# Optimization experiments

Measured on AMD Instinct MI355X. Metric: run time of the kernel, lower is better.

Reference implementation:

```python
import jax, jax.numpy as jnp
import numpy as np

B, N, G = 16, 6000, 256
T = 200                     # TRAIN_ROIS_PER_IMAGE
RATIO = 0.33                # POSITIVE_ROI_RATIO
POS_NUM = int(T * RATIO)    # 66 positive slots
NEG_SLOTS = T - POS_NUM     # 134 negative slots
BBOX_STD = jnp.asarray([0.1, 0.1, 0.2, 0.2], jnp.float32)
EPS = 1e-8


def _rand_boxes(key, b, n):
    # valid [y1,x1,y2,x2] boxes in [0,1]
    k1, k2 = jax.random.split(key)
    tl = jax.random.uniform(k1, (b, n, 2)) * 0.7
    wh = jax.random.uniform(k2, (b, n, 2)) * 0.25 + 0.02
    return jnp.concatenate([tl, tl + wh], axis=-1).astype(jnp.float32)


def setup_inputs() -> dict:
    key = jax.random.key(0)
    k1, k2, k3, k4, k5 = jax.random.split(key, 5)
    rois = _rand_boxes(k1, B, N)
    rois = rois.at[:, N - 1000:].set(0.0)          # zero padding tail (remove_zero_padding)
    gt_boxes = _rand_boxes(k2, B, G)
    gt_ids = jax.random.randint(k3, (B, G), 1, 81, dtype=jnp.int32)
    gt_ids = gt_ids.at[:, G - 32:G - 16].set(-1)   # crowd boxes (ids < 0)
    gt_ids = gt_ids.at[:, G - 16:].set(0)          # padded gt
    gt_boxes = gt_boxes.at[:, G - 16:].set(0.0)
    pos_score = jax.random.uniform(k4, (B, N), dtype=jnp.float32)
    neg_score = jax.random.uniform(k5, (B, N), dtype=jnp.float32)
    return {"rois": rois, "gt_ids": gt_ids, "gt_boxes": gt_boxes,
            "pos_score": pos_score, "neg_score": neg_score}


def _pairwise_iou(a, b):
    # a:[N,4], b:[G,4] -> [N,G]
    y1 = jnp.maximum(a[:, None, 0], b[None, :, 0])
    x1 = jnp.maximum(a[:, None, 1], b[None, :, 1])
    y2 = jnp.minimum(a[:, None, 2], b[None, :, 2])
    x2 = jnp.minimum(a[:, None, 3], b[None, :, 3])
    inter = jnp.clip(y2 - y1, 0.0) * jnp.clip(x2 - x1, 0.0)
    area_a = (a[:, 2] - a[:, 0]) * (a[:, 3] - a[:, 1])
    area_b = (b[:, 2] - b[:, 0]) * (b[:, 3] - b[:, 1])
    union = area_a[:, None] + area_b[None, :] - inter
    return inter / jnp.maximum(union, EPS)


def _bbox_offset(boxes, gt):
    h = jnp.maximum(boxes[:, 2] - boxes[:, 0], EPS)
    w = jnp.maximum(boxes[:, 3] - boxes[:, 1], EPS)
    cy = boxes[:, 0] + 0.5 * h
    cx = boxes[:, 1] + 0.5 * w
    gh = jnp.maximum(gt[:, 2] - gt[:, 0], EPS)
    gw = jnp.maximum(gt[:, 3] - gt[:, 1], EPS)
    gcy = gt[:, 0] + 0.5 * gh
    gcx = gt[:, 1] + 0.5 * gw
    off = jnp.stack([(gcy - cy) / h, (gcx - cx) / w,
                     jnp.log(gh / h), jnp.log(gw / w)], axis=1)
    return off / BBOX_STD


def _per_image(rois, gt_ids, gt_boxes, pos_score, neg_score):
    roi_valid = jnp.any(rois != 0.0, axis=1)        # [N]
    gt_valid = jnp.any(gt_boxes != 0.0, axis=1)     # [G]
    crowd = gt_valid & (gt_ids < 0)
    non_crowd = gt_valid & (gt_ids > 0)

    iou = _pairwise_iou(rois, gt_boxes)             # [N,G]
    iou_nc = jnp.where(non_crowd[None, :], iou, -1.0)
    iou_nc_max = jnp.max(iou_nc, axis=1)
    iou_cr_max = jnp.max(jnp.where(crowd[None, :], iou, 0.0), axis=1)

    pos_mask = roi_valid & (iou_nc_max >= 0.5)
    neg_mask = roi_valid & (iou_nc_max < 0.5) & (iou_cr_max < 0.001)

    # random sampling == sort by iid uniform scores (masked out -> -inf)
    pos_idx = jnp.argsort(-jnp.where(pos_mask, pos_score, -jnp.inf))[:POS_NUM]
    pos_count = jnp.minimum(jnp.sum(pos_mask), POS_NUM).astype(jnp.int32)
    pos_slot_valid = jnp.arange(POS_NUM) < pos_count

    neg_target = (jnp.float32(1.0 / RATIO) * pos_count.astype(jnp.float32)).astype(jnp.int32) - pos_count
    neg_idx = jnp.argsort(-jnp.where(neg_mask, neg_score, -jnp.inf))[:NEG_SLOTS]
    neg_count = jnp.minimum(jnp.sum(neg_mask).astype(jnp.int32),
                            jnp.minimum(neg_target, NEG_SLOTS))
    neg_slot_valid = jnp.arange(NEG_SLOTS) < neg_count

    pos_rois_raw = rois[pos_idx]                                   # [P,4]
    pos_rois = jnp.where(pos_slot_valid[:, None], pos_rois_raw, 0.0)
    neg_rois = jnp.where(neg_slot_valid[:, None], rois[neg_idx], 0.0)

    assign = jnp.argmax(iou_nc[pos_idx], axis=1)                   # gt assignment
    roi_gt_boxes = gt_boxes[assign]
    roi_gt_ids = jnp.where(pos_slot_valid, gt_ids[assign], 0)

    off = _bbox_offset(pos_rois_raw, roi_gt_boxes)
    off = jnp.where(pos_slot_valid[:, None], off, 0.0)

    out_rois = jnp.concatenate([pos_rois, neg_rois], axis=0)       # [T,4]
    out_ids = jnp.pad(roi_gt_ids, (0, NEG_SLOTS))                  # [T]
    out_off = jnp.pad(off, ((0, NEG_SLOTS), (0, 0)))               # [T,4]
    return out_rois, out_ids, out_off


def reference(rois, gt_ids, gt_boxes, pos_score, neg_score):
    return jax.vmap(_per_image)(rois, gt_ids, gt_boxes, pos_score, neg_score)
```

## Files before the change

kernel.cpp:

```cpp
#include <hip/hip_runtime.h>

#define BIMG 16
#define NROI 6000
#define NGT  256
#define TPOS 66
#define TNEG 134
#define TTOT 200
#define EPSF 1e-8f
#define INVALID_SCORE 0xFFFFFFFFu

#define RPB 128
#define UNITSB 47
#define P1_BLOCKS (UNITSB * BIMG)
#define NWAIT (2 * BIMG)
#define NT 256
#define VSLOTS 6
#define CAND_CAP 384

#define MAGIC1 0x9E3779B9u
#define MAGIC2 0x85EBCA77u

typedef unsigned long long u64;
typedef unsigned int u32;
typedef unsigned short u16;

struct P1Shared {
    float4 ncbox[NGT];
    float  ncarea[NGT];
    float4 crbox[NGT];
    float  crarea[NGT];
    u16    gmap[NGT];
    int    wnc[4], wcr[4];
    int    poscnt;
};

struct SelShared {
    u32 hist[2048];
    u32 wtot[4];
    u32 wsuf[4];
    int pick;
    u32 higher;
    u32 pickpop;
    u32 count;
    u64 comp[CAND_CAP];
    int cnt;
    int sel[TNEG];
};

__device__ __forceinline__ void phase1_block(
    int unit,
    const float* __restrict__ rois, const int* __restrict__ gt_ids,
    const float* __restrict__ gt_boxes, const float* __restrict__ pos_score,
    const float* __restrict__ neg_score, u32* __restrict__ pos_s,
    u32* __restrict__ neg_s, u32* __restrict__ assign, u32* __restrict__ flags,
    P1Shared& S)
{
#pragma clang fp contract(off)
    const int b = unit / UNITSB;
    const int u = unit - b * UNITSB;
    const int tid = threadIdx.x;
    const int sub = tid & 1;
    const int r   = tid >> 1;

    if (tid == 0) S.poscnt = 0;

    const int n = u * RPB + r;
    const int ne = min(n, NROI - 1);
    const float4 rb = ((const float4*)rois)[b * NROI + ne];
    float ps_in = 0.f, ns_in = 0.f;
    if (sub == 0) {
        ps_in = pos_score[b * NROI + ne];
        ns_in = neg_score[b * NROI + ne];
    }

    {
        const int g = tid;
        const int lane = g & 63, w = g >> 6;
        float4 gb = ((const float4*)gt_boxes)[b * NGT + g];
        bool valid = (gb.x != 0.f) || (gb.y != 0.f) || (gb.z != 0.f) || (gb.w != 0.f);
        int id = gt_ids[b * NGT + g];
        float area = (gb.z - gb.x) * (gb.w - gb.y);
        bool isnc = valid && (id > 0);
        bool iscr = valid && (id < 0);
        u64 mnc = __ballot(isnc);
        u64 mcr = __ballot(iscr);
        if (lane == 0) { S.wnc[w] = (int)__popcll(mnc); S.wcr[w] = (int)__popcll(mcr); }
        __syncthreads();
        int offnc = 0, offcr = 0;
        for (int j = 0; j < w; ++j) { offnc += S.wnc[j]; offcr += S.wcr[j]; }
        u64 below = (lane == 0) ? 0ull : (~0ull >> (64 - lane));
        if (isnc) {
            int slot = offnc + (int)__popcll(mnc & below);
            S.ncbox[slot] = gb;
            S.ncarea[slot] = area;
            S.gmap[slot] = (u16)g;
        }
        if (iscr) {
            int slot = offcr + (int)__popcll(mcr & below);
            S.crbox[slot] = gb;
            S.crarea[slot] = area;
        }
    }
    __syncthreads();
    const int nccnt = S.wnc[0] + S.wnc[1] + S.wnc[2] + S.wnc[3];
    const int crcnt = S.wcr[0] + S.wcr[1] + S.wcr[2] + S.wcr[3];

    const bool rvalid = (rb.x != 0.f) || (rb.y != 0.f) || (rb.z != 0.f) || (rb.w != 0.f);
    float best = -1.0f;
    int   bsl  = 0;
    float crmax = 0.0f;

    if (rvalid) {
        const float area_a = (rb.z - rb.x) * (rb.w - rb.y);
        const int h  = nccnt >> 1;
        const int i0 = sub ? h : 0;
        const int i1 = sub ? nccnt : h;
#pragma unroll 4
        for (int i = i0; i < i1; ++i) {
            float4 p0 = S.ncbox[i];
            float  ab = S.ncarea[i];
            float y1 = fmaxf(rb.x, p0.x);
            float x1 = fmaxf(rb.y, p0.y);
            float y2 = fminf(rb.z, p0.z);
            float x2 = fminf(rb.w, p0.w);
            float ih = fmaxf(y2 - y1, 0.0f);
            float iw = fmaxf(x2 - x1, 0.0f);
            float inter = ih * iw;
            float uni = fmaxf(area_a + ab - inter, EPSF);
            float iou = inter / uni;
            if (iou > best) { best = iou; bsl = i; }
        }
        const int hc  = crcnt >> 1;
        const int c0i = sub ? hc : 0;
        const int c1i = sub ? crcnt : hc;
#pragma unroll 4
        for (int i = c0i; i < c1i; ++i) {
            float4 p0 = S.crbox[i];
            float  ab = S.crarea[i];
            float y1 = fmaxf(rb.x, p0.x);
            float x1 = fmaxf(rb.y, p0.y);
            float y2 = fminf(rb.z, p0.z);
            float x2 = fminf(rb.w, p0.w);
            float ih = fmaxf(y2 - y1, 0.0f);
            float iw = fmaxf(x2 - x1, 0.0f);
            float inter = ih * iw;
            float uni = fmaxf(area_a + ab - inter, EPSF);
            crmax = fmaxf(crmax, inter / uni);
        }
        float ov = __shfl_xor(best, 1);
        int   os = __shfl_xor(bsl, 1);
        float oc = __shfl_xor(crmax, 1);
        if ((ov > best) || ((ov == best) && (os < bsl))) { best = ov; bsl = os; }
        crmax = fmaxf(crmax, oc);
    }

    u32 ps = INVALID_SCORE, ns = INVALID_SCORE;
    if (rvalid && n < NROI) {
        if (best >= 0.5f)
            ps = __float_as_uint(ps_in);
        if ((best < 0.5f) && (crmax < 0.001f))
            ns = __float_as_uint(ns_in);
    }
    {
        u64 pb = __ballot((sub == 0) && (ps != INVALID_SCORE));
        if ((tid & 63) == 0) atomicAdd(&S.poscnt, (int)__popcll(pb));
    }
    if (sub == 0 && n < NROI) {
        int gsel = (nccnt > 0) ? (int)S.gmap[bsl] : 0;
        __hip_atomic_store(&pos_s[b * NROI + n], ps,
                           __ATOMIC_RELAXED, __HIP_MEMORY_SCOPE_AGENT);
        __hip_atomic_store(&neg_s[b * NROI + n], ns,
                           __ATOMIC_RELAXED, __HIP_MEMORY_SCOPE_AGENT);
        __hip_atomic_store(&assign[b * NROI + n], (u32)gsel,
                           __ATOMIC_RELAXED, __HIP_MEMORY_SCOPE_AGENT);
    }

    __syncthreads();
    if (tid == 0) {
        u32 cnt = (u32)S.poscnt;
        __hip_atomic_store(&flags[2 * unit],     MAGIC1 ^ cnt,
                           __ATOMIC_RELAXED, __HIP_MEMORY_SCOPE_AGENT);
        __hip_atomic_store(&flags[2 * unit + 1], MAGIC2 ^ cnt,
                           __ATOMIC_RELAXED, __HIP_MEMORY_SCOPE_AGENT);
    }
}

__device__ __forceinline__ int radix_select(const u32* __restrict__ src, int K,
                                            int tid, int lane, int w, SelShared* S)
{
    const uint4* src4 = (const uint4*)src;
    int myvalid = 0;
#pragma unroll
    for (int s = 0; s < VSLOTS; ++s) {
        int vi = s * NT + tid;
        uint4 v = src4[vi];
        int base = vi * 4;
        myvalid += (base + 0 < NROI && v.x != INVALID_SCORE);
        myvalid += (base + 1 < NROI && v.y != INVALID_SCORE);
        myvalid += (base + 2 < NROI && v.z != INVALID_SCORE);
        myvalid += (base + 3 < NROI && v.w != INVALID_SCORE);
    }
    for (int off = 1; off < 64; off <<= 1) myvalid += __shfl_xor(myvalid, off);
    if (tid == 0) S->count = 0;
    __syncthreads();
    if (lane == 0) atomicAdd(&S->count, (u32)myvalid);
    __syncthreads();
    const int total = (int)S->count;
    const int K0 = min(K, total);
    if (K0 <= 0) return total;

    int Krem = K0;
    u64 prefix = 0ull, mask = 0ull;
    int cand = total;

    for (int p = 3; p >= 0; --p) {
        if (cand <= CAND_CAP) break;
        const int shift = p * 11;
        for (int i = tid; i < 2048; i += NT) S->hist[i] = 0;
        __syncthreads();
#pragma unroll
        for (int s = 0; s < VSLOTS; ++s) {
            int vi = s * NT + tid;
            uint4 v = src4[vi];
            int base = vi * 4;
            u32 vv[4] = {v.x, v.y, v.z, v.w};
#pragma unroll
            for (int j = 0; j < 4; ++j) {
                int idx = base + j;
                if (idx < NROI && vv[j] != INVALID_SCORE) {
                    u64 kk = ((u64)vv[j] << 13) | (u64)(8191 - idx);
                    if ((kk & mask) == prefix)
                        atomicAdd(&S->hist[(u32)(kk >> shift) & 2047u], 1u);
                }
            }
        }
        __syncthreads();
        u32 local = 0;
#pragma unroll
        for (int j = 0; j < 8; ++j) local += S->hist[8 * tid + j];
        u32 suf = local;
        for (int off = 1; off < 64; off <<= 1) {
            u32 v = __shfl_down(suf, off);
            if (lane + off < 64) suf += v;
        }
        if (lane == 0) S->wtot[w] = suf;
        __syncthreads();
        if (tid < 4) {
            u32 t = 0;
            for (int j = tid + 1; j < 4; ++j) t += S->wtot[j];
            S->wsuf[tid] = t;
        }
        __syncthreads();
        u32 Sincl = suf + S->wsuf[w];
        for (int k2 = 0; k2 < 8; ++k2) {
            u32 h = S->hist[8 * tid + k2];
            u32 Snext = Sincl - h;
            if (Sincl >= (u32)Krem && Snext < (u32)Krem) {
                S->pick = 8 * tid + k2;
                S->higher = Snext;
                S->pickpop = h;
            }
            Sincl = Snext;
        }
        __syncthreads();
        prefix |= ((u64)(u32)S->pick) << shift;
        mask   |= (2047ull << shift);
        Krem   -= (int)S->higher;
        cand    = (K0 - Krem) + (int)S->pickpop;
        __syncthreads();
    }

    if (tid == 0) S->cnt = 0;
    __syncthreads();
#pragma unroll
    for (int s = 0; s < VSLOTS; ++s) {
        int vi = s * NT + tid;
        uint4 v = src4[vi];
        int base = vi * 4;
        u32 vv[4] = {v.x, v.y, v.z, v.w};
#pragma unroll
        for (int j = 0; j < 4; ++j) {
            int idx = base + j;
            if (idx < NROI && vv[j] != INVALID_SCORE) {
                u64 kk = ((u64)vv[j] << 13) | (u64)(8191 - idx);
                if ((kk & mask) >= prefix) {
                    int pos = atomicAdd(&S->cnt, 1);
                    S->comp[pos] = kk;
                }
            }
        }
    }
    __syncthreads();
    const int Cnt = S->cnt;
    const int CntP = (Cnt + 15) & ~15;
    for (int i = Cnt + tid; i < CntP; i += NT) S->comp[i] = 0ull;
    __syncthreads();
    for (int c0 = tid; c0 < Cnt; c0 += NT) {
        u64 kk = S->comp[c0];
        int rank = 0;
        for (int j = 0; j < CntP; j += 16) {
            int r16 = 0;
#pragma unroll
            for (int q = 0; q < 16; ++q) r16 += (S->comp[j + q] > kk);
            rank += r16;
        }
        if (rank < K0) S->sel[rank] = 8191 - (int)(kk & 8191ull);
    }
    __syncthreads();
    return total;
}

__device__ __forceinline__ void phase2_block(
    int wbid,
    const float* __restrict__ rois, const int* __restrict__ gt_ids,
    const float* __restrict__ gt_boxes, const u32* __restrict__ pos_s,
    const u32* __restrict__ neg_s, const u32* __restrict__ assign,
    const u32* __restrict__ flags, float* __restrict__ out, SelShared& S)
{
#pragma clang fp contract(off)
    __shared__ int s_ndone;
    __shared__ int s_psum;
    const int b = wbid >> 1;
    const int side = wbid & 1;
    const int tid = threadIdx.x;
    const int lane = tid & 63;
    const int w = tid >> 6;

    const u32* fb = flags + 2 * (b * UNITSB);
    int mydone = (tid < UNITSB) ? 0 : 1;
    int mycnt = 0;
    for (;;) {
        if (tid == 0) s_ndone = 0;
        __syncthreads();
        if (!mydone) {
            u32 a = __hip_atomic_load(&fb[2 * tid],
                                      __ATOMIC_RELAXED, __HIP_MEMORY_SCOPE_AGENT);
            u32 c = __hip_atomic_load(&fb[2 * tid + 1],
                                      __ATOMIC_RELAXED, __HIP_MEMORY_SCOPE_AGENT);
            u32 ca = a ^ MAGIC1, cb = c ^ MAGIC2;
            if (ca == cb && ca <= (u32)RPB) { mydone = 1; mycnt = (int)ca; }
        }
        int d = mydone;
        for (int off = 1; off < 64; off <<= 1) d += __shfl_xor(d, off);
        if (lane == 0) atomicAdd(&s_ndone, d);
        __syncthreads();
        if (s_ndone == NT) break;
        __builtin_amdgcn_s_sleep(8);
    }
    if (tid == 0) {
        (void)__hip_atomic_load(&fb[0], __ATOMIC_ACQUIRE, __HIP_MEMORY_SCOPE_AGENT);
        s_psum = 0;
    }
    __syncthreads();
    if (tid < UNITSB && mycnt) atomicAdd(&s_psum, mycnt);
    __syncthreads();
    const int pos_total = s_psum;

    float* out_rois = out;
    float* out_ids  = out + BIMG * TTOT * 4;
    float* out_off  = out + BIMG * TTOT * 4 + BIMG * TTOT;

    if (side == 0) {
        radix_select(pos_s + (size_t)b * NROI, TPOS, tid, lane, w, &S);
        const int pos_count = min(pos_total, TPOS);

        if (tid < TPOS) {
            const int base = b * TTOT + tid;
            float4 ro  = make_float4(0.f, 0.f, 0.f, 0.f);
            float  idv = 0.f;
            float4 off = make_float4(0.f, 0.f, 0.f, 0.f);
            if (tid < pos_count) {
                int nn = S.sel[tid];
                float4 rb = ((const float4*)rois)[b * NROI + nn];
                ro = rb;
                int g = (int)assign[b * NROI + nn];
                float4 gb = ((const float4*)gt_boxes)[b * NGT + g];
                idv = (float)gt_ids[b * NGT + g];

                float h  = fmaxf(rb.z - rb.x, EPSF);
                float wd = fmaxf(rb.w - rb.y, EPSF);
                float cy = rb.x + 0.5f * h;
                float cx = rb.y + 0.5f * wd;
                float gh = fmaxf(gb.z - gb.x, EPSF);
                float gw = fmaxf(gb.w - gb.y, EPSF);
                float gcy = gb.x + 0.5f * gh;
                float gcx = gb.y + 0.5f * gw;
                off.x = ((gcy - cy) / h)  / 0.1f;
                off.y = ((gcx - cx) / wd) / 0.1f;
                off.z = logf(gh / h)  / 0.2f;
                off.w = logf(gw / wd) / 0.2f;
            }
            ((float4*)out_rois)[base] = ro;
            out_ids[base] = idv;
            ((float4*)out_off)[base] = off;
        }
    } else {
        const int pos_count = min(pos_total, TPOS);
        const float ratio_inv = (float)(1.0 / 0.33);
        const int neg_target = (int)(ratio_inv * (float)pos_count) - pos_count;

        const int neg_total = radix_select(neg_s + (size_t)b * NROI, TNEG,
                                           tid, lane, w, &S);
        const int neg_count = max(0, min(neg_total, min(neg_target, TNEG)));

        if (tid < TNEG) {
            const int base = b * TTOT + TPOS + tid;
            float4 ro = make_float4(0.f, 0.f, 0.f, 0.f);
            if (tid < neg_count) {
                int nn = S.sel[tid];
                ro = ((const float4*)rois)[b * NROI + nn];
            }
            ((float4*)out_rois)[base] = ro;
            out_ids[base] = 0.f;
            ((float4*)out_off)[base] = make_float4(0.f, 0.f, 0.f, 0.f);
        }
    }
}

__global__ __launch_bounds__(NT, 4)
void fused_kernel(const float* __restrict__ rois,
                  const int* __restrict__ gt_ids,
                  const float* __restrict__ gt_boxes,
                  const float* __restrict__ pos_score,
                  const float* __restrict__ neg_score,
                  u32* __restrict__ pos_s,
                  u32* __restrict__ neg_s,
                  u32* __restrict__ assign,
                  u32* __restrict__ flags,
                  float* __restrict__ out)
{
    constexpr size_t SB = sizeof(P1Shared) > sizeof(SelShared)
                        ? sizeof(P1Shared) : sizeof(SelShared);
    __shared__ __align__(16) char smem[SB];

    if (blockIdx.x >= NWAIT) {
        phase1_block((int)blockIdx.x - NWAIT, rois, gt_ids, gt_boxes, pos_score,
                     neg_score, pos_s, neg_s, assign, flags,
                     *reinterpret_cast<P1Shared*>(smem));
    } else {
        phase2_block((int)blockIdx.x, rois, gt_ids, gt_boxes,
                     pos_s, neg_s, assign, flags, out,
                     *reinterpret_cast<SelShared*>(smem));
    }
}

extern "C" void kernel_launch(void* const* d_in, const int* in_sizes, int n_in,
                              void* d_out, int out_size, void* d_ws, size_t ws_size,
                              hipStream_t stream) {
    const float* rois      = (const float*)d_in[0];
    const int*   gt_ids    = (const int*)d_in[1];
    const float* gt_boxes  = (const float*)d_in[2];
    const float* pos_score = (const float*)d_in[3];
    const float* neg_score = (const float*)d_in[4];
    float* out = (float*)d_out;

    char* ws = (char*)d_ws;
    u32* pos_s  = (u32*)(ws + 0);
    u32* neg_s  = (u32*)(ws + 384000);
    u32* assign = (u32*)(ws + 768000);
    u32* flags  = (u32*)(ws + 1152000);

    fused_kernel<<<NWAIT + P1_BLOCKS, NT, 0, stream>>>(
        rois, gt_ids, gt_boxes, pos_score, neg_score,
        pos_s, neg_s, assign, flags, out);
}
```

Before: 94.33 us.

## Fold selection phase into last two phase-1 blocks per image, drop dedicated waiters

Removes the 32 separate waiter blocks. The last two phase-1 blocks of each image now run their own IoU work first, then spin on the flags and perform the positive/negative radix selection. This frees the slots that waiter blocks held while spinning, and cuts shared memory by recomputing gt areas inline. In exchange the selection starts only after those final blocks finish their phase-1 work, and it relies on all blocks of an image being co-resident to avoid deadlock.

```diff
diff --git a/kernel.cpp b/kernel.cpp
--- a/kernel.cpp
+++ b/kernel.cpp
@@ -12,7 +12,6 @@
 #define RPB 128
 #define UNITSB 47
 #define P1_BLOCKS (UNITSB * BIMG)
-#define NWAIT (2 * BIMG)
 #define NT 256
 #define VSLOTS 6
 #define CAND_CAP 384
@@ -26,9 +25,7 @@
 
 struct P1Shared {
     float4 ncbox[NGT];
-    float  ncarea[NGT];
     float4 crbox[NGT];
-    float  crarea[NGT];
     u16    gmap[NGT];
     int    wnc[4], wcr[4];
     int    poscnt;
@@ -47,18 +44,157 @@
     int sel[TNEG];
 };
 
-__device__ __forceinline__ void phase1_block(
-    int unit,
-    const float* __restrict__ rois, const int* __restrict__ gt_ids,
-    const float* __restrict__ gt_boxes, const float* __restrict__ pos_score,
-    const float* __restrict__ neg_score, u32* __restrict__ pos_s,
-    u32* __restrict__ neg_s, u32* __restrict__ assign, u32* __restrict__ flags,
-    P1Shared& S)
+__device__ __forceinline__ int radix_select(const u32* __restrict__ src, int K,
+                                            int tid, int lane, int w, SelShared* S)
+{
+    const uint4* src4 = (const uint4*)src;
+    int myvalid = 0;
+#pragma unroll
+    for (int s = 0; s < VSLOTS; ++s) {
+        int vi = s * NT + tid;
+        uint4 v = src4[vi];
+        int base = vi * 4;
+        myvalid += (base + 0 < NROI && v.x != INVALID_SCORE);
+        myvalid += (base + 1 < NROI && v.y != INVALID_SCORE);
+        myvalid += (base + 2 < NROI && v.z != INVALID_SCORE);
+        myvalid += (base + 3 < NROI && v.w != INVALID_SCORE);
+    }
+    for (int off = 1; off < 64; off <<= 1) myvalid += __shfl_xor(myvalid, off);
+    if (tid == 0) S->count = 0;
+    __syncthreads();
+    if (lane == 0) atomicAdd(&S->count, (u32)myvalid);
+    __syncthreads();
+    const int total = (int)S->count;
+    const int K0 = min(K, total);
+    if (K0 <= 0) return total;
+
+    int Krem = K0;
+    u64 prefix = 0ull, mask = 0ull;
+    int cand = total;
+
+    for (int p = 3; p >= 0; --p) {
+        if (cand <= CAND_CAP) break;
+        const int shift = p * 11;
+        for (int i = tid; i < 2048; i += NT) S->hist[i] = 0;
+        __syncthreads();
+#pragma unroll
+        for (int s = 0; s < VSLOTS; ++s) {
+            int vi = s * NT + tid;
+            uint4 v = src4[vi];
+            int base = vi * 4;
+            u32 vv[4] = {v.x, v.y, v.z, v.w};
+#pragma unroll
+            for (int j = 0; j < 4; ++j) {
+                int idx = base + j;
+                if (idx < NROI && vv[j] != INVALID_SCORE) {
+                    u64 kk = ((u64)vv[j] << 13) | (u64)(8191 - idx);
+                    if ((kk & mask) == prefix)
+                        atomicAdd(&S->hist[(u32)(kk >> shift) & 2047u], 1u);
+                }
+            }
+        }
+        __syncthreads();
+        u32 local = 0;
+#pragma unroll
+        for (int j = 0; j < 8; ++j) local += S->hist[8 * tid + j];
+        u32 suf = local;
+        for (int off = 1; off < 64; off <<= 1) {
+            u32 v = __shfl_down(suf, off);
+            if (lane + off < 64) suf += v;
+        }
+        if (lane == 0) S->wtot[w] = suf;
+        __syncthreads();
+        if (tid < 4) {
+            u32 t = 0;
+            for (int j = tid + 1; j < 4; ++j) t += S->wtot[j];
+            S->wsuf[tid] = t;
+        }
+        __syncthreads();
+        u32 Sincl = suf + S->wsuf[w];
+        for (int k2 = 0; k2 < 8; ++k2) {
+            u32 h = S->hist[8 * tid + k2];
+            u32 Snext = Sincl - h;
+            if (Sincl >= (u32)Krem && Snext < (u32)Krem) {
+                S->pick = 8 * tid + k2;
+                S->higher = Snext;
+                S->pickpop = h;
+            }
+            Sincl = Snext;
+        }
+        __syncthreads();
+        prefix |= ((u64)(u32)S->pick) << shift;
+        mask   |= (2047ull << shift);
+        Krem   -= (int)S->higher;
+        cand    = (K0 - Krem) + (int)S->pickpop;
+        __syncthreads();
+    }
+
+    if (tid == 0) S->cnt = 0;
+    __syncthreads();
+#pragma unroll
+    for (int s = 0; s < VSLOTS; ++s) {
+        int vi = s * NT + tid;
+        uint4 v = src4[vi];
+        int base = vi * 4;
+        u32 vv[4] = {v.x, v.y, v.z, v.w};
+#pragma unroll
+        for (int j = 0; j < 4; ++j) {
+            int idx = base + j;
+            if (idx < NROI && vv[j] != INVALID_SCORE) {
+                u64 kk = ((u64)vv[j] << 13) | (u64)(8191 - idx);
+                if ((kk & mask) >= prefix) {
+                    int pos = atomicAdd(&S->cnt, 1);
+                    S->comp[pos] = kk;
+                }
+            }
+        }
+    }
+    __syncthreads();
+    const int Cnt = S->cnt;
+    const int CntP = (Cnt + 15) & ~15;
+    for (int i = Cnt + tid; i < CntP; i += NT) S->comp[i] = 0ull;
+    __syncthreads();
+    for (int c0 = tid; c0 < Cnt; c0 += NT) {
+        u64 kk = S->comp[c0];
+        int rank = 0;
+        for (int j = 0; j < CntP; j += 16) {
+            int r16 = 0;
+#pragma unroll
+            for (int q = 0; q < 16; ++q) r16 += (S->comp[j + q] > kk);
+            rank += r16;
+        }
+        if (rank < K0) S->sel[rank] = 8191 - (int)(kk & 8191ull);
+    }
+    __syncthreads();
+    return total;
+}
+
+__global__ __launch_bounds__(NT, 4)
+void fused_kernel(const float* __restrict__ rois,
+                  const int* __restrict__ gt_ids,
+                  const float* __restrict__ gt_boxes,
+                  const float* __restrict__ pos_score,
+                  const float* __restrict__ neg_score,
+                  u32* __restrict__ pos_s,
+                  u32* __restrict__ neg_s,
+                  u32* __restrict__ assign,
+                  u32* __restrict__ flags,
+                  float* __restrict__ out)
 {
 #pragma clang fp contract(off)
+    constexpr size_t SB = sizeof(P1Shared) > sizeof(SelShared)
+                        ? sizeof(P1Shared) : sizeof(SelShared);
+    __shared__ __align__(16) char smem[SB];
+    __shared__ int s_ndone;
+    __shared__ int s_psum;
+    P1Shared& S = *reinterpret_cast<P1Shared*>(smem);
+
+    const int unit = (int)blockIdx.x;
     const int b = unit / UNITSB;
     const int u = unit - b * UNITSB;
     const int tid = threadIdx.x;
+    const int lane = tid & 63;
+    const int w = tid >> 6;
     const int sub = tid & 1;
     const int r   = tid >> 1;
 
@@ -75,11 +211,9 @@
 
     {
         const int g = tid;
-        const int lane = g & 63, w = g >> 6;
         float4 gb = ((const float4*)gt_boxes)[b * NGT + g];
         bool valid = (gb.x != 0.f) || (gb.y != 0.f) || (gb.z != 0.f) || (gb.w != 0.f);
         int id = gt_ids[b * NGT + g];
-        float area = (gb.z - gb.x) * (gb.w - gb.y);
         bool isnc = valid && (id > 0);
         bool iscr = valid && (id < 0);
         u64 mnc = __ballot(isnc);
@@ -92,13 +226,11 @@
         if (isnc) {
             int slot = offnc + (int)__popcll(mnc & below);
             S.ncbox[slot] = gb;
-            S.ncarea[slot] = area;
             S.gmap[slot] = (u16)g;
         }
         if (iscr) {
             int slot = offcr + (int)__popcll(mcr & below);
             S.crbox[slot] = gb;
-            S.crarea[slot] = area;
         }
     }
     __syncthreads();
@@ -118,7 +250,7 @@
 #pragma unroll 4
         for (int i = i0; i < i1; ++i) {
             float4 p0 = S.ncbox[i];
-            float  ab = S.ncarea[i];
+            float ab = (p0.z - p0.x) * (p0.w - p0.y);
             float y1 = fmaxf(rb.x, p0.x);
             float x1 = fmaxf(rb.y, p0.y);
             float y2 = fminf(rb.z, p0.z);
@@ -136,7 +268,7 @@
 #pragma unroll 4
         for (int i = c0i; i < c1i; ++i) {
             float4 p0 = S.crbox[i];
-            float  ab = S.crarea[i];
+            float ab = (p0.z - p0.x) * (p0.w - p0.y);
             float y1 = fmaxf(rb.x, p0.x);
             float x1 = fmaxf(rb.y, p0.y);
             float y2 = fminf(rb.z, p0.z);
@@ -163,7 +295,7 @@
     }
     {
         u64 pb = __ballot((sub == 0) && (ps != INVALID_SCORE));
-        if ((tid & 63) == 0) atomicAdd(&S.poscnt, (int)__popcll(pb));
+        if (lane == 0) atomicAdd(&S.poscnt, (int)__popcll(pb));
     }
     if (sub == 0 && n < NROI) {
         int gsel = (nccnt > 0) ? (int)S.gmap[bsl] : 0;
@@ -183,148 +315,9 @@
         __hip_atomic_store(&flags[2 * unit + 1], MAGIC2 ^ cnt,
                            __ATOMIC_RELAXED, __HIP_MEMORY_SCOPE_AGENT);
     }
-}
-
-__device__ __forceinline__ int radix_select(const u32* __restrict__ src, int K,
-                                            int tid, int lane, int w, SelShared* S)
-{
-    const uint4* src4 = (const uint4*)src;
-    int myvalid = 0;
-#pragma unroll
-    for (int s = 0; s < VSLOTS; ++s) {
-        int vi = s * NT + tid;
-        uint4 v = src4[vi];
-        int base = vi * 4;
-        myvalid += (base + 0 < NROI && v.x != INVALID_SCORE);
-        myvalid += (base + 1 < NROI && v.y != INVALID_SCORE);
-        myvalid += (base + 2 < NROI && v.z != INVALID_SCORE);
-        myvalid += (base + 3 < NROI && v.w != INVALID_SCORE);
-    }
-    for (int off = 1; off < 64; off <<= 1) myvalid += __shfl_xor(myvalid, off);
-    if (tid == 0) S->count = 0;
-    __syncthreads();
-    if (lane == 0) atomicAdd(&S->count, (u32)myvalid);
-    __syncthreads();
-    const int total = (int)S->count;
-    const int K0 = min(K, total);
-    if (K0 <= 0) return total;
-
-    int Krem = K0;
-    u64 prefix = 0ull, mask = 0ull;
-    int cand = total;
-
-    for (int p = 3; p >= 0; --p) {
-        if (cand <= CAND_CAP) break;
-        const int shift = p * 11;
-        for (int i = tid; i < 2048; i += NT) S->hist[i] = 0;
-        __syncthreads();
-#pragma unroll
-        for (int s = 0; s < VSLOTS; ++s) {
-            int vi = s * NT + tid;
-            uint4 v = src4[vi];
-            int base = vi * 4;
-            u32 vv[4] = {v.x, v.y, v.z, v.w};
-#pragma unroll
-            for (int j = 0; j < 4; ++j) {
-                int idx = base + j;
-                if (idx < NROI && vv[j] != INVALID_SCORE) {
-                    u64 kk = ((u64)vv[j] << 13) | (u64)(8191 - idx);
-                    if ((kk & mask) == prefix)
-                        atomicAdd(&S->hist[(u32)(kk >> shift) & 2047u], 1u);
-                }
-            }
-        }
-        __syncthreads();
-        u32 local = 0;
-#pragma unroll
-        for (int j = 0; j < 8; ++j) local += S->hist[8 * tid + j];
-        u32 suf = local;
-        for (int off = 1; off < 64; off <<= 1) {
-            u32 v = __shfl_down(suf, off);
-            if (lane + off < 64) suf += v;
-        }
-        if (lane == 0) S->wtot[w] = suf;
-        __syncthreads();
-        if (tid < 4) {
-            u32 t = 0;
-            for (int j = tid + 1; j < 4; ++j) t += S->wtot[j];
-            S->wsuf[tid] = t;
-        }
-        __syncthreads();
-        u32 Sincl = suf + S->wsuf[w];
-        for (int k2 = 0; k2 < 8; ++k2) {
-            u32 h = S->hist[8 * tid + k2];
-            u32 Snext = Sincl - h;
-            if (Sincl >= (u32)Krem && Snext < (u32)Krem) {
-                S->pick = 8 * tid + k2;
-                S->higher = Snext;
-                S->pickpop = h;
-            }
-            Sincl = Snext;
-        }
-        __syncthreads();
-        prefix |= ((u64)(u32)S->pick) << shift;
-        mask   |= (2047ull << shift);
-        Krem   -= (int)S->higher;
-        cand    = (K0 - Krem) + (int)S->pickpop;
-        __syncthreads();
-    }
-
-    if (tid == 0) S->cnt = 0;
-    __syncthreads();
-#pragma unroll
-    for (int s = 0; s < VSLOTS; ++s) {
-        int vi = s * NT + tid;
-        uint4 v = src4[vi];
-        int base = vi * 4;
-        u32 vv[4] = {v.x, v.y, v.z, v.w};
-#pragma unroll
-        for (int j = 0; j < 4; ++j) {
-            int idx = base + j;
-            if (idx < NROI && vv[j] != INVALID_SCORE) {
-                u64 kk = ((u64)vv[j] << 13) | (u64)(8191 - idx);
-                if ((kk & mask) >= prefix) {
-                    int pos = atomicAdd(&S->cnt, 1);
-                    S->comp[pos] = kk;
-                }
-            }
-        }
-    }
-    __syncthreads();
-    const int Cnt = S->cnt;
-    const int CntP = (Cnt + 15) & ~15;
-    for (int i = Cnt + tid; i < CntP; i += NT) S->comp[i] = 0ull;
-    __syncthreads();
-    for (int c0 = tid; c0 < Cnt; c0 += NT) {
-        u64 kk = S->comp[c0];
-        int rank = 0;
-        for (int j = 0; j < CntP; j += 16) {
-            int r16 = 0;
-#pragma unroll
-            for (int q = 0; q < 16; ++q) r16 += (S->comp[j + q] > kk);
-            rank += r16;
-        }
-        if (rank < K0) S->sel[rank] = 8191 - (int)(kk & 8191ull);
-    }
-    __syncthreads();
-    return total;
-}
-
-__device__ __forceinline__ void phase2_block(
-    int wbid,
-    const float* __restrict__ rois, const int* __restrict__ gt_ids,
-    const float* __restrict__ gt_boxes, const u32* __restrict__ pos_s,
-    const u32* __restrict__ neg_s, const u32* __restrict__ assign,
-    const u32* __restrict__ flags, float* __restrict__ out, SelShared& S)
-{
-#pragma clang fp contract(off)
-    __shared__ int s_ndone;
-    __shared__ int s_psum;
-    const int b = wbid >> 1;
-    const int side = wbid & 1;
-    const int tid = threadIdx.x;
-    const int lane = tid & 63;
-    const int w = tid >> 6;
+
+    if (u < UNITSB - 2) return;
+    const int side = (u == UNITSB - 1) ? 1 : 0;
 
     const u32* fb = flags + 2 * (b * UNITSB);
     int mydone = (tid < UNITSB) ? 0 : 1;
@@ -356,12 +349,14 @@
     __syncthreads();
     const int pos_total = s_psum;
 
+    SelShared& Q = *reinterpret_cast<SelShared*>(smem);
+
     float* out_rois = out;
     float* out_ids  = out + BIMG * TTOT * 4;
     float* out_off  = out + BIMG * TTOT * 4 + BIMG * TTOT;
 
     if (side == 0) {
-        radix_select(pos_s + (size_t)b * NROI, TPOS, tid, lane, w, &S);
+        radix_select(pos_s + (size_t)b * NROI, TPOS, tid, lane, w, &Q);
         const int pos_count = min(pos_total, TPOS);
 
         if (tid < TPOS) {
@@ -370,17 +365,17 @@
             float  idv = 0.f;
             float4 off = make_float4(0.f, 0.f, 0.f, 0.f);
             if (tid < pos_count) {
-                int nn = S.sel[tid];
-                float4 rb = ((const float4*)rois)[b * NROI + nn];
-                ro = rb;
+                int nn = Q.sel[tid];
+                float4 rb2 = ((const float4*)rois)[b * NROI + nn];
+                ro = rb2;
                 int g = (int)assign[b * NROI + nn];
                 float4 gb = ((const float4*)gt_boxes)[b * NGT + g];
                 idv = (float)gt_ids[b * NGT + g];
 
-                float h  = fmaxf(rb.z - rb.x, EPSF);
-                float wd = fmaxf(rb.w - rb.y, EPSF);
-                float cy = rb.x + 0.5f * h;
-                float cx = rb.y + 0.5f * wd;
+                float h  = fmaxf(rb2.z - rb2.x, EPSF);
+                float wd = fmaxf(rb2.w - rb2.y, EPSF);
+                float cy = rb2.x + 0.5f * h;
+                float cx = rb2.y + 0.5f * wd;
                 float gh = fmaxf(gb.z - gb.x, EPSF);
                 float gw = fmaxf(gb.w - gb.y, EPSF);
                 float gcy = gb.x + 0.5f * gh;
@@ -400,47 +395,20 @@
         const int neg_target = (int)(ratio_inv * (float)pos_count) - pos_count;
 
         const int neg_total = radix_select(neg_s + (size_t)b * NROI, TNEG,
-                                           tid, lane, w, &S);
+                                           tid, lane, w, &Q);
         const int neg_count = max(0, min(neg_total, min(neg_target, TNEG)));
 
         if (tid < TNEG) {
             const int base = b * TTOT + TPOS + tid;
             float4 ro = make_float4(0.f, 0.f, 0.f, 0.f);
             if (tid < neg_count) {
-                int nn = S.sel[tid];
+                int nn = Q.sel[tid];
                 ro = ((const float4*)rois)[b * NROI + nn];
             }
             ((float4*)out_rois)[base] = ro;
             out_ids[base] = 0.f;
             ((float4*)out_off)[base] = make_float4(0.f, 0.f, 0.f, 0.f);
         }
-    }
-}
-
-__global__ __launch_bounds__(NT, 4)
-void fused_kernel(const float* __restrict__ rois,
-                  const int* __restrict__ gt_ids,
-                  const float* __restrict__ gt_boxes,
-                  const float* __restrict__ pos_score,
-                  const float* __restrict__ neg_score,
-                  u32* __restrict__ pos_s,
-                  u32* __restrict__ neg_s,
-                  u32* __restrict__ assign,
-                  u32* __restrict__ flags,
-                  float* __restrict__ out)
-{
-    constexpr size_t SB = sizeof(P1Shared) > sizeof(SelShared)
-                        ? sizeof(P1Shared) : sizeof(SelShared);
-    __shared__ __align__(16) char smem[SB];
-
-    if (blockIdx.x >= NWAIT) {
-        phase1_block((int)blockIdx.x - NWAIT, rois, gt_ids, gt_boxes, pos_score,
-                     neg_score, pos_s, neg_s, assign, flags,
-                     *reinterpret_cast<P1Shared*>(smem));
-    } else {
-        phase2_block((int)blockIdx.x, rois, gt_ids, gt_boxes,
-                     pos_s, neg_s, assign, flags, out,
-                     *reinterpret_cast<SelShared*>(smem));
     }
 }
 
@@ -460,7 +428,7 @@
     u32* assign = (u32*)(ws + 768000);
     u32* flags  = (u32*)(ws + 1152000);
 
-    fused_kernel<<<NWAIT + P1_BLOCKS, NT, 0, stream>>>(
+    fused_kernel<<<P1_BLOCKS, NT, 0, stream>>>(
         rois, gt_ids, gt_boxes, pos_score, neg_score,
         pos_s, neg_s, assign, flags, out);
 }
```

Result: no change. 96.11 us (+1.9%).
